# Kernel optimization log

Hardware: AMD Instinct MI355X
Metric: run time of the kernel (lower is better)

The kernel has to match this reference:

```python
import jax, jax.numpy as jnp
import numpy as np


def setup_inputs() -> dict:
    key = jax.random.key(0)
    ks = jax.random.split(key, 6)
    B, N_in, N_out, D_in, D_out, S = 64, 195, 778, 256, 128, 9
    nnz = 3 * N_out
    x = jax.random.normal(ks[0], (B, N_in, D_in), dtype=jnp.float32)
    # upsample transform: each output vertex receives 3 weighted source verts
    row = jnp.repeat(jnp.arange(N_out, dtype=jnp.int64), 3)
    col = jax.random.randint(ks[1], (nnz,), 0, N_in).astype(jnp.int64)
    value = jax.random.uniform(ks[2], (nnz,), dtype=jnp.float32)
    indices = jax.random.randint(ks[3], (N_out, S), 0, N_out).astype(jnp.int64)
    W = jax.random.normal(ks[4], (D_in * S, D_out), dtype=jnp.float32) * 0.02
    b = jnp.zeros((D_out,), dtype=jnp.float32)
    return {"x": x, "row": row, "col": col, "value": value,
            "indices": indices, "W": W, "b": b}


def reference(x, row, col, value, indices, W, b):
    B, N_in, D = x.shape
    N_out, S = indices.shape
    # Pool: gather source verts, scale by barycentric weight, scatter-add
    msg = x[:, col, :] * value[None, :, None]                # (B, nnz, D)
    pooled = jnp.zeros((B, N_out, D), x.dtype).at[:, row, :].add(msg)
    # SpiralConv: gather spiral neighborhood, flatten, linear
    g = pooled[:, indices.reshape(-1), :].reshape(B, N_out, S * D)
    out = jnp.einsum('bnk,ko->bno', g, W) + b                # (B, N_out, D_out)
    return jax.nn.relu(out)
```

## Files before the change

### kernel.cpp

```cpp
#include <hip/hip_runtime.h>
#include <hip/hip_bf16.h>
#include <stdint.h>

#define N_IN 195
#define N_OUT 778
#define D_IN 256
#define D_OUTC 128
#define NS 9
#define KTOT 2304
#define MM 49792
#define BM 128
#define BK 64
#define NWG 389
#define POOL_BLOCKS 12448
#define WT_BLOCKS 1152

using short8  = __attribute__((ext_vector_type(8))) short;
using short4v = __attribute__((ext_vector_type(4))) short;
using f32x4   = __attribute__((ext_vector_type(4))) float;

__device__ __forceinline__ void gload16(const void* g, void* l) {
  __builtin_amdgcn_global_load_lds(
      (const __attribute__((address_space(1))) uint32_t*)g,
      (__attribute__((address_space(3))) uint32_t*)l, 16, 0, 0);
}

__device__ __forceinline__ unsigned short f2bf(float f) {
  uint32_t u = __float_as_uint(f);
  return (unsigned short)((u + 0x7FFFu + ((u >> 16) & 1u)) >> 16);
}

__global__ __launch_bounds__(256) void prep_kernel(
    const float* __restrict__ x, const int* __restrict__ col,
    const float* __restrict__ value, const float* __restrict__ W,
    unsigned short* __restrict__ pooled, unsigned short* __restrict__ Wt) {
  int bid = blockIdx.x;
  if (bid < POOL_BLOCKS) {
    int m = bid * 4 + (threadIdx.x >> 6);
    int lane = threadIdx.x & 63;
    int b = (unsigned)m / N_OUT;
    int n = m - b * N_OUT;
    int j = 3 * n;
    int c0 = col[j], c1 = col[j + 1], c2 = col[j + 2];
    float v0 = value[j], v1 = value[j + 1], v2 = value[j + 2];
    const float4* x0 = (const float4*)(x + ((size_t)b * N_IN + c0) * D_IN);
    const float4* x1 = (const float4*)(x + ((size_t)b * N_IN + c1) * D_IN);
    const float4* x2 = (const float4*)(x + ((size_t)b * N_IN + c2) * D_IN);
    float4 a0 = x0[lane], a1 = x1[lane], a2 = x2[lane];
    short4v pk;
    pk[0] = (short)f2bf(v0 * a0.x + v1 * a1.x + v2 * a2.x);
    pk[1] = (short)f2bf(v0 * a0.y + v1 * a1.y + v2 * a2.y);
    pk[2] = (short)f2bf(v0 * a0.z + v1 * a1.z + v2 * a2.z);
    pk[3] = (short)f2bf(v0 * a0.w + v1 * a1.w + v2 * a2.w);
    ((short4v*)(pooled + (size_t)m * D_IN))[lane] = pk;
  } else {
    int idx = (bid - POOL_BLOCKS) * 256 + threadIdx.x;
    int o = idx / KTOT, k = idx - o * KTOT;
    Wt[idx] = f2bf(W[(size_t)k * D_OUTC + o]);
  }
}

__global__ __launch_bounds__(512, 4) void gemm_kernel(
    const unsigned short* __restrict__ pooled,
    const unsigned short* __restrict__ Wt,
    const int* __restrict__ indices,
    const float* __restrict__ bias,
    float* __restrict__ out) {
  __shared__ unsigned short Asm[2][BM * BK];
  __shared__ unsigned short Bsm[2][D_OUTC * BK];

  const int tid = threadIdx.x;
  const int wave = tid >> 6, lane = tid & 63;
  const int wr = wave >> 1, wc = wave & 1;

  const int xcd = blockIdx.x & 7, loc = blockIdx.x >> 3;
  const int q8 = NWG >> 3, r8 = NWG & 7;
  const int wg = (xcd < r8 ? xcd * (q8 + 1) : r8 * (q8 + 1) + (xcd - r8) * q8) + loc;
  const int bm = wg * BM;

  const int srow = tid >> 3;
  const int sc = ((tid & 7) ^ (srow & 7)) * 8;
  int nn[2]; size_t gb[2];
  const unsigned short* wtrow[2];
  #pragma unroll
  for (int i = 0; i < 2; ++i) {
    int r = i * 64 + srow;
    int m = bm + r;
    int b = (unsigned)m / N_OUT;
    nn[i] = m - b * N_OUT;
    gb[i] = (size_t)b * N_OUT;
    wtrow[i] = Wt + (size_t)r * KTOT + sc;
  }
  char* AsmB = (char*)&Asm[0][0];
  char* BsmB = (char*)&Bsm[0][0];

  int gc[2], gn[2];
  #pragma unroll
  for (int i = 0; i < 2; ++i) gc[i] = indices[nn[i] * NS + 0];

  f32x4 acc[2][4];
  #pragma unroll
  for (int i = 0; i < 2; ++i)
    #pragma unroll
    for (int j = 0; j < 4; ++j) acc[i][j] = f32x4{0.f, 0.f, 0.f, 0.f};

  auto stage = [&](int buf, int s, int q, const int* g) {
    const int bofs = buf * 16384;
    const int kq = s * 256 + q * 64;
    #pragma unroll
    for (int i = 0; i < 2; ++i) {
      const unsigned short* srcA =
          pooled + (((gb[i] + (size_t)g[i]) << 8) + q * 64 + sc);
      gload16(srcA, AsmB + bofs + i * 8192 + tid * 16);
      gload16(wtrow[i] + kq, BsmB + bofs + i * 8192 + tid * 16);
    }
  };

  auto compute = [&](int buf) {
    const char* Ab = AsmB + buf * 16384;
    const char* Bb = BsmB + buf * 16384;
    #pragma unroll
    for (int h = 0; h < 2; ++h) {
      short8 af[2], bf[4];
      const int cb = h * 64 + (lane >> 4) * 16;
      #pragma unroll
      for (int i = 0; i < 2; ++i) {
        int r = wr * 32 + i * 16 + (lane & 15);
        af[i] = *(const short8*)(Ab + r * 128 + (cb ^ ((r & 7) << 4)));
      }
      #pragma unroll
      for (int j = 0; j < 4; ++j) {
        int o = wc * 64 + j * 16 + (lane & 15);
        bf[j] = *(const short8*)(Bb + o * 128 + (cb ^ ((o & 7) << 4)));
      }
      __builtin_amdgcn_s_setprio(1);
      #pragma unroll
      for (int i = 0; i < 2; ++i)
        #pragma unroll
        for (int j = 0; j < 4; ++j)
          acc[i][j] = __builtin_amdgcn_mfma_f32_16x16x32_bf16(
              af[i], bf[j], acc[i][j], 0, 0, 0);
      __builtin_amdgcn_s_setprio(0);
    }
  };

  stage(0, 0, 0, gc);
  __syncthreads();

  for (int s = 0; s < NS; ++s) {
    #pragma unroll
    for (int q = 0; q < 4; ++q) {
      int buf = (s * 4 + q) & 1;
      if (q == 0 && s < NS - 1) {
        #pragma unroll
        for (int i = 0; i < 2; ++i) gn[i] = indices[nn[i] * NS + s + 1];
      }
      if (q < 3)            stage(buf ^ 1, s, q + 1, gc);
      else if (s < NS - 1)  stage(buf ^ 1, s + 1, 0, gn);
      compute(buf);
      __syncthreads();
    }
    #pragma unroll
    for (int i = 0; i < 2; ++i) gc[i] = gn[i];
  }

  #pragma unroll
  for (int j = 0; j < 4; ++j) {
    int colo = wc * 64 + j * 16 + (lane & 15);
    float bo = bias[colo];
    #pragma unroll
    for (int i = 0; i < 2; ++i) {
      int rb = bm + wr * 32 + i * 16 + (lane >> 4) * 4;
      #pragma unroll
      for (int q = 0; q < 4; ++q) {
        int row = rb + q;
        out[(size_t)row * D_OUTC + colo] = fmaxf(acc[i][j][q] + bo, 0.f);
      }
    }
  }
}

extern "C" void kernel_launch(void* const* d_in, const int* in_sizes, int n_in,
                              void* d_out, int out_size, void* d_ws, size_t ws_size,
                              hipStream_t stream) {
  const float* x       = (const float*)d_in[0];
  const int*   col     = (const int*)d_in[2];
  const float* value   = (const float*)d_in[3];
  const int*   indices = (const int*)d_in[4];
  const float* W       = (const float*)d_in[5];
  const float* bias    = (const float*)d_in[6];
  float* out           = (float*)d_out;

  unsigned short* pooled = (unsigned short*)d_ws;
  unsigned short* Wt = (unsigned short*)((char*)d_ws + (size_t)MM * D_IN * 2);

  prep_kernel<<<POOL_BLOCKS + WT_BLOCKS, 256, 0, stream>>>(x, col, value, W,
                                                           pooled, Wt);
  gemm_kernel<<<NWG, 512, 0, stream>>>(pooled, Wt, indices, bias, out);
}
```

Measured before the change: 62.03 us.

## Pre-swizzle weights into MFMA fragment layout and load B directly to registers

The prep kernel now writes the bf16 weights in per-lane MFMA fragment order, so each lane can fetch its B operand as one 16-byte load. The GEMM no longer stages B through LDS; each wave reads its fragments straight from global memory (mostly L2-resident) into registers every k-step. This halves LDS usage and LDS traffic, and prep launches fewer blocks. The cost is exposed global-load latency on B within each iteration, since it is not prefetched ahead, plus redundant B reads across the waves that share columns.

```diff
diff --git a/kernel.cpp b/kernel.cpp
--- a/kernel.cpp
+++ b/kernel.cpp
@@ -13,7 +13,7 @@
 #define BK 64
 #define NWG 389
 #define POOL_BLOCKS 12448
-#define WT_BLOCKS 1152
+#define BF_BLOCKS 144
 
 using short8  = __attribute__((ext_vector_type(8))) short;
 using short4v = __attribute__((ext_vector_type(4))) short;
@@ -33,7 +33,7 @@
 __global__ __launch_bounds__(256) void prep_kernel(
     const float* __restrict__ x, const int* __restrict__ col,
     const float* __restrict__ value, const float* __restrict__ W,
-    unsigned short* __restrict__ pooled, unsigned short* __restrict__ Wt) {
+    unsigned short* __restrict__ pooled, unsigned short* __restrict__ Bfrag) {
   int bid = blockIdx.x;
   if (bid < POOL_BLOCKS) {
     int m = bid * 4 + (threadIdx.x >> 6);
@@ -55,19 +55,26 @@
     ((short4v*)(pooled + (size_t)m * D_IN))[lane] = pk;
   } else {
     int idx = (bid - POOL_BLOCKS) * 256 + threadIdx.x;
-    int o = idx / KTOT, k = idx - o * KTOT;
-    Wt[idx] = f2bf(W[(size_t)k * D_OUTC + o]);
+    int lane = idx & 63;
+    int cf = (idx >> 6) & 7;
+    int kb = idx >> 9;
+    int kbase = kb * 32 + (lane >> 4) * 8;
+    int o = cf * 16 + (lane & 15);
+    short8 pk;
+    #pragma unroll
+    for (int e = 0; e < 8; ++e)
+      pk[e] = (short)f2bf(W[(size_t)(kbase + e) * D_OUTC + o]);
+    *(short8*)(Bfrag + (size_t)idx * 8) = pk;
   }
 }
 
 __global__ __launch_bounds__(512, 4) void gemm_kernel(
     const unsigned short* __restrict__ pooled,
-    const unsigned short* __restrict__ Wt,
+    const unsigned short* __restrict__ Bfrag,
     const int* __restrict__ indices,
     const float* __restrict__ bias,
     float* __restrict__ out) {
   __shared__ unsigned short Asm[2][BM * BK];
-  __shared__ unsigned short Bsm[2][D_OUTC * BK];
 
   const int tid = threadIdx.x;
   const int wave = tid >> 6, lane = tid & 63;
@@ -81,7 +88,6 @@
   const int srow = tid >> 3;
   const int sc = ((tid & 7) ^ (srow & 7)) * 8;
   int nn[2]; size_t gb[2];
-  const unsigned short* wtrow[2];
   #pragma unroll
   for (int i = 0; i < 2; ++i) {
     int r = i * 64 + srow;
@@ -89,10 +95,10 @@
     int b = (unsigned)m / N_OUT;
     nn[i] = m - b * N_OUT;
     gb[i] = (size_t)b * N_OUT;
-    wtrow[i] = Wt + (size_t)r * KTOT + sc;
   }
   char* AsmB = (char*)&Asm[0][0];
-  char* BsmB = (char*)&Bsm[0][0];
+
+  const unsigned short* bfbase = Bfrag + ((size_t)wc * 4 * 64 + lane) * 8;
 
   int gc[2], gn[2];
   #pragma unroll
@@ -104,60 +110,65 @@
     #pragma unroll
     for (int j = 0; j < 4; ++j) acc[i][j] = f32x4{0.f, 0.f, 0.f, 0.f};
 
-  auto stage = [&](int buf, int s, int q, const int* g) {
+  auto stageA = [&](int buf, int s, int q, const int* g) {
     const int bofs = buf * 16384;
-    const int kq = s * 256 + q * 64;
     #pragma unroll
     for (int i = 0; i < 2; ++i) {
       const unsigned short* srcA =
           pooled + (((gb[i] + (size_t)g[i]) << 8) + q * 64 + sc);
       gload16(srcA, AsmB + bofs + i * 8192 + tid * 16);
-      gload16(wtrow[i] + kq, BsmB + bofs + i * 8192 + tid * 16);
     }
   };
 
-  auto compute = [&](int buf) {
+  auto loadB = [&](short8 bf[2][4], int p) {
+    #pragma unroll
+    for (int h = 0; h < 2; ++h) {
+      const unsigned short* kb = bfbase + (size_t)(p * 2 + h) * 8 * 64 * 8;
+      #pragma unroll
+      for (int j = 0; j < 4; ++j)
+        bf[h][j] = *(const short8*)(kb + (size_t)j * 64 * 8);
+    }
+  };
+
+  auto compute = [&](int buf, const short8 bf[2][4]) {
     const char* Ab = AsmB + buf * 16384;
-    const char* Bb = BsmB + buf * 16384;
     #pragma unroll
     for (int h = 0; h < 2; ++h) {
-      short8 af[2], bf[4];
+      short8 af[2];
       const int cb = h * 64 + (lane >> 4) * 16;
       #pragma unroll
       for (int i = 0; i < 2; ++i) {
         int r = wr * 32 + i * 16 + (lane & 15);
         af[i] = *(const short8*)(Ab + r * 128 + (cb ^ ((r & 7) << 4)));
       }
-      #pragma unroll
-      for (int j = 0; j < 4; ++j) {
-        int o = wc * 64 + j * 16 + (lane & 15);
-        bf[j] = *(const short8*)(Bb + o * 128 + (cb ^ ((o & 7) << 4)));
-      }
       __builtin_amdgcn_s_setprio(1);
       #pragma unroll
       for (int i = 0; i < 2; ++i)
         #pragma unroll
         for (int j = 0; j < 4; ++j)
           acc[i][j] = __builtin_amdgcn_mfma_f32_16x16x32_bf16(
-              af[i], bf[j], acc[i][j], 0, 0, 0);
+              af[i], bf[h][j], acc[i][j], 0, 0, 0);
       __builtin_amdgcn_s_setprio(0);
     }
   };
 
-  stage(0, 0, 0, gc);
+  stageA(0, 0, 0, gc);
   __syncthreads();
 
   for (int s = 0; s < NS; ++s) {
     #pragma unroll
     for (int q = 0; q < 4; ++q) {
-      int buf = (s * 4 + q) & 1;
+      int p = s * 4 + q;
+      int buf = p & 1;
+      short8 bf[2][4];
+      loadB(bf, p);
       if (q == 0 && s < NS - 1) {
         #pragma unroll
         for (int i = 0; i < 2; ++i) gn[i] = indices[nn[i] * NS + s + 1];
       }
-      if (q < 3)            stage(buf ^ 1, s, q + 1, gc);
-      else if (s < NS - 1)  stage(buf ^ 1, s + 1, 0, gn);
-      compute(buf);
+      if (q < 3)            stageA(buf ^ 1, s, q + 1, gc);
+      else if (s < NS - 1)  stageA(buf ^ 1, s + 1, 0, gn);
+      compute(buf, bf);
       __syncthreads();
     }
     #pragma unroll
@@ -192,9 +203,9 @@
   float* out           = (float*)d_out;
 
   unsigned short* pooled = (unsigned short*)d_ws;
-  unsigned short* Wt = (unsigned short*)((char*)d_ws + (size_t)MM * D_IN * 2);
-
-  prep_kernel<<<POOL_BLOCKS + WT_BLOCKS, 256, 0, stream>>>(x, col, value, W,
-                                                           pooled, Wt);
-  gemm_kernel<<<NWG, 512, 0, stream>>>(pooled, Wt, indices, bias, out);
-}
+  unsigned short* Bfrag = (unsigned short*)((char*)d_ws + (size_t)MM * D_IN * 2);
+
+  prep_kernel<<<POOL_BLOCKS + BF_BLOCKS, 256, 0, stream>>>(x, col, value, W,
+                                                           pooled, Bfrag);
+  gemm_kernel<<<NWG, 512, 0, stream>>>(pooled, Bfrag, indices, bias, out);
+}
```

Result: slower. 81.26 us (+31.0%).

## Double GEMM row tile to 256 and pre-convert x to bf16

Applied to the files above, without the earlier changes.

The GEMM M-tile grows from 128 to 256 rows, which halves the workgroup count to 195. Each wave now holds a 64x64 accumulator, so every loaded W tile is reused across more rows, and out-of-range rows are guarded. A separate kernel converts x to bf16 first, so the pooling gather reads half as many bytes per source row. The cost is an extra launch plus a full write and read of x, lower occupancy (launch bounds 512,2), and fewer workgroups than the MI355X has compute units.

```diff
diff --git a/kernel.cpp b/kernel.cpp
--- a/kernel.cpp
+++ b/kernel.cpp
@@ -9,14 +9,15 @@
 #define NS 9
 #define KTOT 2304
 #define MM 49792
-#define BM 128
+#define BM 256
 #define BK 64
-#define NWG 389
-#define POOL_BLOCKS 12448
+#define NWG 195
+#define XE 3194880
+#define XCVT_BLOCKS 1560
+#define POOL_BLOCKS 6224
 #define WT_BLOCKS 1152
 
 using short8  = __attribute__((ext_vector_type(8))) short;
-using short4v = __attribute__((ext_vector_type(4))) short;
 using f32x4   = __attribute__((ext_vector_type(4))) float;
 
 __device__ __forceinline__ void gload16(const void* g, void* l) {
@@ -29,30 +30,49 @@
   uint32_t u = __float_as_uint(f);
   return (unsigned short)((u + 0x7FFFu + ((u >> 16) & 1u)) >> 16);
 }
+__device__ __forceinline__ float bf2f(unsigned short s) {
+  return __uint_as_float(((uint32_t)s) << 16);
+}
+
+__global__ __launch_bounds__(256) void xcvt_kernel(
+    const float* __restrict__ x, unsigned short* __restrict__ xh) {
+  int i = (blockIdx.x * 256 + threadIdx.x) * 8;
+  float4 a = *(const float4*)(x + i);
+  float4 b = *(const float4*)(x + i + 4);
+  short8 pk;
+  pk[0] = (short)f2bf(a.x); pk[1] = (short)f2bf(a.y);
+  pk[2] = (short)f2bf(a.z); pk[3] = (short)f2bf(a.w);
+  pk[4] = (short)f2bf(b.x); pk[5] = (short)f2bf(b.y);
+  pk[6] = (short)f2bf(b.z); pk[7] = (short)f2bf(b.w);
+  *(short8*)(xh + i) = pk;
+}
 
 __global__ __launch_bounds__(256) void prep_kernel(
-    const float* __restrict__ x, const int* __restrict__ col,
+    const unsigned short* __restrict__ xh, const int* __restrict__ col,
     const float* __restrict__ value, const float* __restrict__ W,
     unsigned short* __restrict__ pooled, unsigned short* __restrict__ Wt) {
   int bid = blockIdx.x;
   if (bid < POOL_BLOCKS) {
-    int m = bid * 4 + (threadIdx.x >> 6);
-    int lane = threadIdx.x & 63;
+    int m = bid * 8 + (threadIdx.x >> 5);
+    int t = threadIdx.x & 31;
     int b = (unsigned)m / N_OUT;
     int n = m - b * N_OUT;
     int j = 3 * n;
     int c0 = col[j], c1 = col[j + 1], c2 = col[j + 2];
     float v0 = value[j], v1 = value[j + 1], v2 = value[j + 2];
-    const float4* x0 = (const float4*)(x + ((size_t)b * N_IN + c0) * D_IN);
-    const float4* x1 = (const float4*)(x + ((size_t)b * N_IN + c1) * D_IN);
-    const float4* x2 = (const float4*)(x + ((size_t)b * N_IN + c2) * D_IN);
-    float4 a0 = x0[lane], a1 = x1[lane], a2 = x2[lane];
-    short4v pk;
-    pk[0] = (short)f2bf(v0 * a0.x + v1 * a1.x + v2 * a2.x);
-    pk[1] = (short)f2bf(v0 * a0.y + v1 * a1.y + v2 * a2.y);
-    pk[2] = (short)f2bf(v0 * a0.z + v1 * a1.z + v2 * a2.z);
-    pk[3] = (short)f2bf(v0 * a0.w + v1 * a1.w + v2 * a2.w);
-    ((short4v*)(pooled + (size_t)m * D_IN))[lane] = pk;
+    const short8* x0 = (const short8*)(xh + ((size_t)b * N_IN + c0) * D_IN);
+    const short8* x1 = (const short8*)(xh + ((size_t)b * N_IN + c1) * D_IN);
+    const short8* x2 = (const short8*)(xh + ((size_t)b * N_IN + c2) * D_IN);
+    short8 a0 = x0[t], a1 = x1[t], a2 = x2[t];
+    short8 pk;
+    #pragma unroll
+    for (int e = 0; e < 8; ++e) {
+      float f = v0 * bf2f((unsigned short)a0[e]) +
+                v1 * bf2f((unsigned short)a1[e]) +
+                v2 * bf2f((unsigned short)a2[e]);
+      pk[e] = (short)f2bf(f);
+    }
+    ((short8*)(pooled + (size_t)m * D_IN))[t] = pk;
   } else {
     int idx = (bid - POOL_BLOCKS) * 256 + threadIdx.x;
     int o = idx / KTOT, k = idx - o * KTOT;
@@ -60,7 +80,7 @@
   }
 }
 
-__global__ __launch_bounds__(512, 4) void gemm_kernel(
+__global__ __launch_bounds__(512, 2) void gemm_kernel(
     const unsigned short* __restrict__ pooled,
     const unsigned short* __restrict__ Wt,
     const int* __restrict__ indices,
@@ -80,52 +100,55 @@
 
   const int srow = tid >> 3;
   const int sc = ((tid & 7) ^ (srow & 7)) * 8;
-  int nn[2]; size_t gb[2];
-  const unsigned short* wtrow[2];
-  #pragma unroll
-  for (int i = 0; i < 2; ++i) {
+  int nn[4]; size_t gb[4];
+  #pragma unroll
+  for (int i = 0; i < 4; ++i) {
     int r = i * 64 + srow;
-    int m = bm + r;
+    int m = bm + r; if (m >= MM) m = MM - 1;
     int b = (unsigned)m / N_OUT;
     nn[i] = m - b * N_OUT;
     gb[i] = (size_t)b * N_OUT;
-    wtrow[i] = Wt + (size_t)r * KTOT + sc;
-  }
+  }
+  const unsigned short* wtrow[2];
+  #pragma unroll
+  for (int i = 0; i < 2; ++i)
+    wtrow[i] = Wt + (size_t)(i * 64 + srow) * KTOT + sc;
   char* AsmB = (char*)&Asm[0][0];
   char* BsmB = (char*)&Bsm[0][0];
 
-  int gc[2], gn[2];
-  #pragma unroll
-  for (int i = 0; i < 2; ++i) gc[i] = indices[nn[i] * NS + 0];
-
-  f32x4 acc[2][4];
-  #pragma unroll
-  for (int i = 0; i < 2; ++i)
+  int gc[4], gn[4];
+  #pragma unroll
+  for (int i = 0; i < 4; ++i) gc[i] = indices[nn[i] * NS + 0];
+
+  f32x4 acc[4][4];
+  #pragma unroll
+  for (int i = 0; i < 4; ++i)
     #pragma unroll
     for (int j = 0; j < 4; ++j) acc[i][j] = f32x4{0.f, 0.f, 0.f, 0.f};
 
   auto stage = [&](int buf, int s, int q, const int* g) {
-    const int bofs = buf * 16384;
     const int kq = s * 256 + q * 64;
     #pragma unroll
-    for (int i = 0; i < 2; ++i) {
+    for (int i = 0; i < 4; ++i) {
       const unsigned short* srcA =
           pooled + (((gb[i] + (size_t)g[i]) << 8) + q * 64 + sc);
-      gload16(srcA, AsmB + bofs + i * 8192 + tid * 16);
-      gload16(wtrow[i] + kq, BsmB + bofs + i * 8192 + tid * 16);
-    }
+      gload16(srcA, AsmB + buf * 32768 + i * 8192 + tid * 16);
+    }
+    #pragma unroll
+    for (int i = 0; i < 2; ++i)
+      gload16(wtrow[i] + kq, BsmB + buf * 16384 + i * 8192 + tid * 16);
   };
 
   auto compute = [&](int buf) {
-    const char* Ab = AsmB + buf * 16384;
+    const char* Ab = AsmB + buf * 32768;
     const char* Bb = BsmB + buf * 16384;
     #pragma unroll
     for (int h = 0; h < 2; ++h) {
-      short8 af[2], bf[4];
+      short8 af[4], bf[4];
       const int cb = h * 64 + (lane >> 4) * 16;
       #pragma unroll
-      for (int i = 0; i < 2; ++i) {
-        int r = wr * 32 + i * 16 + (lane & 15);
+      for (int i = 0; i < 4; ++i) {
+        int r = wr * 64 + i * 16 + (lane & 15);
         af[i] = *(const short8*)(Ab + r * 128 + (cb ^ ((r & 7) << 4)));
       }
       #pragma unroll
@@ -135,7 +158,7 @@
       }
       __builtin_amdgcn_s_setprio(1);
       #pragma unroll
-      for (int i = 0; i < 2; ++i)
+      for (int i = 0; i < 4; ++i)
         #pragma unroll
         for (int j = 0; j < 4; ++j)
           acc[i][j] = __builtin_amdgcn_mfma_f32_16x16x32_bf16(
@@ -153,7 +176,7 @@
       int buf = (s * 4 + q) & 1;
       if (q == 0 && s < NS - 1) {
         #pragma unroll
-        for (int i = 0; i < 2; ++i) gn[i] = indices[nn[i] * NS + s + 1];
+        for (int i = 0; i < 4; ++i) gn[i] = indices[nn[i] * NS + s + 1];
       }
       if (q < 3)            stage(buf ^ 1, s, q + 1, gc);
       else if (s < NS - 1)  stage(buf ^ 1, s + 1, 0, gn);
@@ -161,7 +184,7 @@
       __syncthreads();
     }
     #pragma unroll
-    for (int i = 0; i < 2; ++i) gc[i] = gn[i];
+    for (int i = 0; i < 4; ++i) gc[i] = gn[i];
   }
 
   #pragma unroll
@@ -169,12 +192,12 @@
     int colo = wc * 64 + j * 16 + (lane & 15);
     float bo = bias[colo];
     #pragma unroll
-    for (int i = 0; i < 2; ++i) {
-      int rb = bm + wr * 32 + i * 16 + (lane >> 4) * 4;
+    for (int i = 0; i < 4; ++i) {
+      int rb = bm + wr * 64 + i * 16 + (lane >> 4) * 4;
       #pragma unroll
       for (int q = 0; q < 4; ++q) {
         int row = rb + q;
-        out[(size_t)row * D_OUTC + colo] = fmaxf(acc[i][j][q] + bo, 0.f);
+        if (row < MM) out[(size_t)row * D_OUTC + colo] = fmaxf(acc[i][j][q] + bo, 0.f);
       }
     }
   }
@@ -192,9 +215,12 @@
   float* out           = (float*)d_out;
 
   unsigned short* pooled = (unsigned short*)d_ws;
-  unsigned short* Wt = (unsigned short*)((char*)d_ws + (size_t)MM * D_IN * 2);
-
-  prep_kernel<<<POOL_BLOCKS + WT_BLOCKS, 256, 0, stream>>>(x, col, value, W,
+  unsigned short* Wt  = (unsigned short*)((char*)d_ws + (size_t)MM * D_IN * 2);
+  unsigned short* xh  = (unsigned short*)((char*)d_ws + (size_t)MM * D_IN * 2
+                                          + (size_t)D_OUTC * KTOT * 2);
+
+  xcvt_kernel<<<XCVT_BLOCKS, 256, 0, stream>>>(x, xh);
+  prep_kernel<<<POOL_BLOCKS + WT_BLOCKS, 256, 0, stream>>>(xh, col, value, W,
                                                            pooled, Wt);
   gemm_kernel<<<NWG, 512, 0, stream>>>(pooled, Wt, indices, bias, out);
 }
```

New measurement: 73.83 us. 1.19x slower.
